# Optimization experiments

Measured on AMD Instinct MI355X. Metric: run time of the kernel, lower is better.

Reference implementation:

```python
import jax, jax.numpy as jnp
import numpy as np

ALPHA = 32.0
RANK = 16
SCALE = ALPHA / RANK


def setup_inputs() -> dict:
    key = jax.random.key(0)
    k1, k2, k3, k4, k5 = jax.random.split(key, 5)
    B, S, D_IN, D_OUT, N = 4, 2048, 4096, 4096, 8
    x = jax.random.normal(k1, (B, S, D_IN), dtype=jnp.float32)
    routing_w = jax.random.uniform(k2, (B, N), dtype=jnp.float32)
    W_base = jax.random.normal(k3, (D_OUT, D_IN), dtype=jnp.float32) * 0.02
    lora_down = jax.random.normal(k4, (N, RANK, D_IN), dtype=jnp.float32) * 0.02
    lora_up = jax.random.normal(k5, (N, D_OUT, RANK), dtype=jnp.float32) * 0.02
    return {"x": x, "routing_w": routing_w, "W_base": W_base,
            "lora_down": lora_down, "lora_up": lora_up}


def reference(x, routing_w, W_base, lora_down, lora_up):
    # base linear: [B,S,D_in] @ [D_out,D_in]^T -> [B,S,D_out]
    base_out = jnp.einsum('bsi,oi->bso', x, W_base)
    # per-expert LoRA down-proj: [B,S,D_in] x [N,R,D_in] -> [B,N,S,R]
    down = jnp.einsum('bsi,nri->bnsr', x, lora_down)
    # up-proj + scale: [B,N,S,R] x [N,D_out,R] -> [B,N,S,D_out]
    up = jnp.einsum('bnsr,nor->bnso', down, lora_up) * SCALE
    # routing-weighted sum over experts: [B,N] x [B,N,S,D_out] -> [B,S,D_out]
    adapter_out = jnp.einsum('bn,bnso->bso', routing_w, up)
    return base_out + adapter_out
```

## Files before the change

kernel.cpp:

```cpp
#include <hip/hip_runtime.h>
#include <hip/hip_bf16.h>
#include <stdint.h>

#define TOK    8192
#define DIN    4096
#define DOUT   4096
#define NEXP   8
#define RK     16
#define NRANK  128
#define KE     4224
#define SEQB   2048
#define LSCALE 2.0f
#define KSPLIT 4
#define KSLICE (DIN / KSPLIT)

typedef __attribute__((ext_vector_type(8))) short bf8_t;
typedef __attribute__((ext_vector_type(4))) float f4_t;

__device__ __forceinline__ void async_copy16(const void* g, void* l) {
  __builtin_amdgcn_global_load_lds((const __attribute__((address_space(1))) void*)g,
                                   (__attribute__((address_space(3))) void*)l,
                                   16, 0, 0);
}

__device__ __forceinline__ ushort f2bf(float f) {
  __hip_bfloat16 h = __float2bfloat16(f);
  return *reinterpret_cast<ushort*>(&h);
}

#define R0 (TOK * DIN / 8)
#define R1 (DOUT * DIN / 8)
#define R2 (DOUT * NEXP * 2)
#define R3 (NRANK * DIN / 8)
#define RTOT (R0 + R1 + R2 + R3)

__global__ __launch_bounds__(256)
void cvt_all_kernel(const float* __restrict__ x, const float* __restrict__ wb,
                    const float* __restrict__ lu, const float* __restrict__ ld,
                    ushort* __restrict__ Xe, ushort* __restrict__ Wc,
                    ushort* __restrict__ Ldb) {
  int i = blockIdx.x * 256 + threadIdx.x;
  const float* src;
  ushort* dst;
  if (i < R0) {
    int t = i >> 9;
    int c = (i & 511) * 8;
    src = x + (size_t)t * DIN + c;
    dst = Xe + (size_t)t * KE + c;
  } else if (i < R0 + R1) {
    int j = i - R0;
    int t = j >> 9;
    int c = (j & 511) * 8;
    src = wb + (size_t)t * DIN + c;
    dst = Wc + (size_t)t * KE + c;
  } else if (i < R0 + R1 + R2) {
    int j = i - (R0 + R1);
    int o = j >> 4;
    int rem = j & 15;
    int n = rem >> 1;
    int half = rem & 1;
    src = lu + ((size_t)n * DOUT + o) * RK + half * 8;
    dst = Wc + (size_t)o * KE + DIN + n * RK + half * 8;
  } else {
    int j = i - (R0 + R1 + R2);
    src = ld + (size_t)j * 8;
    dst = Ldb + (size_t)j * 8;
  }
  const float4* s = reinterpret_cast<const float4*>(src);
  float4 a = s[0], b = s[1];
  union { ushort u[8]; uint4 v; } o;
  o.u[0]=f2bf(a.x); o.u[1]=f2bf(a.y); o.u[2]=f2bf(a.z); o.u[3]=f2bf(a.w);
  o.u[4]=f2bf(b.x); o.u[5]=f2bf(b.y); o.u[6]=f2bf(b.z); o.u[7]=f2bf(b.w);
  *reinterpret_cast<uint4*>(dst) = o.v;
}

template<int KLEN, int LDB, int MODE>
__global__ __launch_bounds__(256)
void gemm128(const ushort* __restrict__ A,
             const ushort* __restrict__ Bm,
             float* __restrict__ C) {
  __shared__ __align__(16) ushort As[128 * 32];
  __shared__ __align__(16) ushort Bs[128 * 32];

  const int tid  = threadIdx.x;
  const int wave = tid >> 6;
  const int lane = tid & 63;

  int bm, bn;
  if (MODE == 0) {
    int bid = blockIdx.x;
    int xcd = bid & 7;
    int idx = bid >> 3;
    int nt  = xcd * 4 + (idx & 3);
    int mt  = idx >> 2;
    bm = mt * 128;
    bn = nt * 128;
  } else {
    bm = blockIdx.y * 128;
    bn = blockIdx.x * 128;
  }
  const int wm = wave & 1, wn = wave >> 1;

  f4_t acc[4][4];
#pragma unroll
  for (int i = 0; i < 4; i++)
#pragma unroll
    for (int j = 0; j < 4; j++) acc[i][j] = (f4_t){0.f, 0.f, 0.f, 0.f};

  const int f0 = tid * 8;
  const int r0 = f0 >> 5, c0 = f0 & 31;
  const int f1 = (256 + tid) * 8;
  const int r1 = f1 >> 5, c1 = f1 & 31;
  const int l0 = (wave << 6) * 8;
  const int l1 = (256 + (wave << 6)) * 8;

  const ushort* Ar = As + (wm * 64 + (lane & 15)) * 32 + (lane >> 4) * 8;
  const ushort* Br = Bs + (wn * 64 + (lane & 15)) * 32 + (lane >> 4) * 8;

  const int kbase = (MODE == 1) ? blockIdx.z * KSLICE : 0;
  const int kend  = kbase + KLEN;

  for (int k0 = kbase; k0 < kend; k0 += 32) {
    __syncthreads();
    async_copy16(A  + (size_t)(bm + r0) * KE  + k0 + c0, (void*)(As + l0));
    async_copy16(A  + (size_t)(bm + r1) * KE  + k0 + c1, (void*)(As + l1));
    async_copy16(Bm + (size_t)(bn + r0) * LDB + k0 + c0, (void*)(Bs + l0));
    async_copy16(Bm + (size_t)(bn + r1) * LDB + k0 + c1, (void*)(Bs + l1));
    __syncthreads();
    bf8_t av[4], bv[4];
#pragma unroll
    for (int i = 0; i < 4; i++) av[i] = *(const bf8_t*)(Ar + i * 16 * 32);
#pragma unroll
    for (int j = 0; j < 4; j++) bv[j] = *(const bf8_t*)(Br + j * 16 * 32);
#pragma unroll
    for (int i = 0; i < 4; i++)
#pragma unroll
      for (int j = 0; j < 4; j++)
        acc[i][j] = __builtin_amdgcn_mfma_f32_16x16x32_bf16(av[i], bv[j], acc[i][j], 0, 0, 0);
  }

  if (MODE == 0) {
#pragma unroll
    for (int i = 0; i < 4; i++) {
      int row = bm + wm * 64 + i * 16 + (lane >> 4) * 4;
#pragma unroll
      for (int j = 0; j < 4; j++) {
        int col = bn + wn * 64 + j * 16 + (lane & 15);
#pragma unroll
        for (int rr = 0; rr < 4; rr++)
          C[(size_t)(row + rr) * DOUT + col] = acc[i][j][rr];
      }
    }
  } else {
    float* Dz = C + (size_t)blockIdx.z * TOK * NRANK;
#pragma unroll
    for (int i = 0; i < 4; i++) {
      int row = bm + wm * 64 + i * 16 + (lane >> 4) * 4;
#pragma unroll
      for (int j = 0; j < 4; j++) {
        int col = wn * 64 + j * 16 + (lane & 15);
#pragma unroll
        for (int rr = 0; rr < 4; rr++)
          Dz[(size_t)(row + rr) * NRANK + col] = acc[i][j][rr];
      }
    }
  }
}

__global__ void scale_store_kernel(const float* __restrict__ D32,
                                   const float* __restrict__ rw,
                                   ushort* __restrict__ Xe) {
  int i = blockIdx.x * 256 + threadIdx.x;
  int t = i >> 5;
  int g = (i & 31) * 4;
  size_t base = (size_t)t * NRANK + g;
  const size_t ss = (size_t)TOK * NRANK;
  float4 a = *reinterpret_cast<const float4*>(D32 + base);
  float4 b = *reinterpret_cast<const float4*>(D32 + ss + base);
  float4 c = *reinterpret_cast<const float4*>(D32 + 2 * ss + base);
  float4 d = *reinterpret_cast<const float4*>(D32 + 3 * ss + base);
  int n = g >> 4;
  int bb = t / SEQB;
  float s = rw[bb * NEXP + n] * LSCALE;
  union { ushort u[4]; uint2 v; } o;
  o.u[0] = f2bf((a.x + b.x + c.x + d.x) * s);
  o.u[1] = f2bf((a.y + b.y + c.y + d.y) * s);
  o.u[2] = f2bf((a.z + b.z + c.z + d.z) * s);
  o.u[3] = f2bf((a.w + b.w + c.w + d.w) * s);
  *reinterpret_cast<uint2*>(Xe + (size_t)t * KE + DIN + g) = o.v;
}

#define BK32  32
#define NT132 (KE / BK32)

__global__ __launch_bounds__(512, 2)
void gemm256(const ushort* __restrict__ A, const ushort* __restrict__ Bm,
             float* __restrict__ C) {
  __shared__ __align__(16) ushort As[4][256 * 32];
  __shared__ __align__(16) ushort Bs[4][256 * 32];

  const int tid  = threadIdx.x;
  const int w    = tid >> 6;
  const int lane = tid & 63;
  const int wm   = w >> 2;
  const int wn   = w & 3;

  const int bid = blockIdx.x;
  const int xg  = bid & 7;
  const int jj  = bid >> 3;
  const int bm  = (((xg & 3) << 3) + (jj & 7)) << 8;
  const int bn  = (((xg >> 2) << 3) + (jj >> 3)) << 8;

  f4_t acc[8][4];
#pragma unroll
  for (int i = 0; i < 8; ++i)
#pragma unroll
    for (int q = 0; q < 4; ++q) acc[i][q] = (f4_t){0.f, 0.f, 0.f, 0.f};

  const int frow = lane & 15;
  const int cbs  = (((lane >> 4) ^ (frow >> 1)) << 4);
  const int ar0  = wm * 128;
  const int br0  = wn * 64;

  const int sxr = (lane >> 3) << 4;
  const int t0  = (w << 10) + (lane << 4);
  const int l0b = t0 ^ sxr;
  const int l1b = (t0 + 8192) ^ sxr;
  const size_t goff0 = (size_t)(l0b >> 6) * KE + ((l0b & 63) >> 1);
  const size_t goff1 = (size_t)(l1b >> 6) * KE + ((l1b & 63) >> 1);
  const int ld0 = (w << 9);
  const int ld1 = (w << 9) + 4096;

  const ushort* Ap = A  + (size_t)bm * KE;
  const ushort* Bp = Bm + (size_t)bn * KE;

#define STAGE_A256(kt, buf) do {                                   \
    const ushort* cp_ = Ap + (size_t)(kt) * BK32;                  \
    async_copy16(cp_ + goff0, (void*)(As[buf] + ld0));             \
    async_copy16(cp_ + goff1, (void*)(As[buf] + ld1));             \
  } while (0)
#define STAGE_B256(kt, buf) do {                                   \
    const ushort* cp_ = Bp + (size_t)(kt) * BK32;                  \
    async_copy16(cp_ + goff0, (void*)(Bs[buf] + ld0));             \
    async_copy16(cp_ + goff1, (void*)(Bs[buf] + ld1));             \
  } while (0)
#define RD_A(s_, mh, f_) (*(const bf8_t*)((const char*)As[s_] + \
    (((ar0 + (mh) * 64 + (f_) * 16 + frow) << 6) ^ cbs)))
#define RD_B(s_, g_) (*(const bf8_t*)((const char*)Bs[s_] + \
    (((br0 + (g_) * 16 + frow) << 6) ^ cbs)))

  STAGE_A256(0, 0); STAGE_B256(0, 0);
  STAGE_A256(1, 1); STAGE_B256(1, 1);
  STAGE_A256(2, 2); STAGE_B256(2, 2);
  asm volatile("s_waitcnt vmcnt(4)" ::: "memory");
  __builtin_amdgcn_s_barrier();

  bf8_t fA0[2][4], fA1[2][4], fB[2][4];
#pragma unroll
  for (int f = 0; f < 4; ++f) fA0[0][f] = RD_A(0, 0, f);
#pragma unroll
  for (int g = 0; g < 4; ++g) fB[0][g]  = RD_B(0, g);

  for (int t2 = 0; t2 < NT132; t2 += 2) {
#pragma unroll
    for (int u = 0; u < 2; ++u) {
      const int T  = t2 + u;
      const int b  = T & 3;
      const int b1 = (T + 1) & 3;
      const int sb = (T + 3) & 3;

      __builtin_amdgcn_s_setprio(1);
#pragma unroll
      for (int f = 0; f < 4; ++f) fA1[u][f] = RD_A(b, 1, f);
      if (T + 3 < NT132) STAGE_A256(T + 3, sb);
#pragma unroll
      for (int f = 0; f < 4; ++f)
#pragma unroll
        for (int g = 0; g < 4; ++g)
          acc[f][g] = __builtin_amdgcn_mfma_f32_16x16x32_bf16(fA0[u][f], fB[u][g], acc[f][g], 0, 0, 0);
      __builtin_amdgcn_s_setprio(0);
      __builtin_amdgcn_s_barrier();

      __builtin_amdgcn_s_setprio(1);
      if (T + 1 < NT132) {
#pragma unroll
        for (int f = 0; f < 4; ++f) fA0[u ^ 1][f] = RD_A(b1, 0, f);
#pragma unroll
        for (int g = 0; g < 4; ++g) fB[u ^ 1][g]  = RD_B(b1, g);
      }
      if (T + 3 < NT132) STAGE_B256(T + 3, sb);
#pragma unroll
      for (int f = 0; f < 4; ++f)
#pragma unroll
        for (int g = 0; g < 4; ++g)
          acc[4 + f][g] = __builtin_amdgcn_mfma_f32_16x16x32_bf16(fA1[u][f], fB[u][g], acc[4 + f][g], 0, 0, 0);
      __builtin_amdgcn_s_setprio(0);
      if (T < NT132 - 4) asm volatile("s_waitcnt vmcnt(4)" ::: "memory");
      else               asm volatile("s_waitcnt vmcnt(0)" ::: "memory");
      __builtin_amdgcn_s_barrier();
    }
  }

#pragma unroll
  for (int i = 0; i < 8; ++i) {
    int row = bm + wm * 128 + i * 16 + (lane >> 4) * 4;
#pragma unroll
    for (int q = 0; q < 4; ++q) {
      int col = bn + wn * 64 + q * 16 + (lane & 15);
#pragma unroll
      for (int rr = 0; rr < 4; ++rr)
        C[(size_t)(row + rr) * DOUT + col] = acc[i][q][rr];
    }
  }
#undef STAGE_A256
#undef STAGE_B256
#undef RD_A
#undef RD_B
}

extern "C" void kernel_launch(void* const* d_in, const int* in_sizes, int n_in,
                              void* d_out, int out_size, void* d_ws, size_t ws_size,
                              hipStream_t stream) {
  const float* x  = (const float*)d_in[0];
  const float* rw = (const float*)d_in[1];
  const float* wb = (const float*)d_in[2];
  const float* ld = (const float*)d_in[3];
  const float* lu = (const float*)d_in[4];
  float* out = (float*)d_out;

  ushort* Xe  = (ushort*)d_ws;
  ushort* Wc  = Xe + (size_t)TOK * KE;
  ushort* Ldb = Wc + (size_t)DOUT * KE;
  float*  D32 = (float*)(Ldb + (size_t)NRANK * DIN);

  cvt_all_kernel<<<RTOT / 256, 256, 0, stream>>>(x, wb, lu, ld, Xe, Wc, Ldb);

  gemm128<KSLICE, DIN, 1><<<dim3(1, TOK / 128, KSPLIT), 256, 0, stream>>>(Xe, Ldb, D32);
  scale_store_kernel<<<TOK * NRANK / 4 / 256, 256, 0, stream>>>(D32, rw, Xe);
  gemm256<<<dim3((TOK / 256) * (DOUT / 256)), 512, 0, stream>>>(Xe, Wc, out);
}
```

Baseline: 558.5 us.

## Fuse x bf16 conversion and split-K reduction into the LoRA down-projection kernel

The fp32 x conversion moves out of the standalone convert kernel and into the down-projection GEMM. That GEMM now loads x as fp32, converts it to bf16 in registers, and writes it both to LDS and to the extended Xe buffer. The separate scale/store kernel is removed: the last split-K block for each row tile, detected with an atomic counter, sums the partials, applies the routing scale and writes the result into Xe. This saves one full pass over x and a kernel launch. In exchange it adds synchronous global loads in the GEMM loop, a memset, and atomic and threadfence synchronisation.

```diff
diff --git a/kernel.cpp b/kernel.cpp
--- a/kernel.cpp
+++ b/kernel.cpp
@@ -28,33 +28,25 @@
   return *reinterpret_cast<ushort*>(&h);
 }
 
-#define R0 (TOK * DIN / 8)
-#define R1 (DOUT * DIN / 8)
-#define R2 (DOUT * NEXP * 2)
-#define R3 (NRANK * DIN / 8)
-#define RTOT (R0 + R1 + R2 + R3)
+#define RR1 (DOUT * DIN / 8)
+#define RR2 (DOUT * NEXP * 2)
+#define RR3 (NRANK * DIN / 8)
+#define RRTOT (RR1 + RR2 + RR3)
 
 __global__ __launch_bounds__(256)
-void cvt_all_kernel(const float* __restrict__ x, const float* __restrict__ wb,
-                    const float* __restrict__ lu, const float* __restrict__ ld,
-                    ushort* __restrict__ Xe, ushort* __restrict__ Wc,
-                    ushort* __restrict__ Ldb) {
+void cvt_rest_kernel(const float* __restrict__ wb, const float* __restrict__ lu,
+                     const float* __restrict__ ld,
+                     ushort* __restrict__ Wc, ushort* __restrict__ Ldb) {
   int i = blockIdx.x * 256 + threadIdx.x;
   const float* src;
   ushort* dst;
-  if (i < R0) {
+  if (i < RR1) {
     int t = i >> 9;
     int c = (i & 511) * 8;
-    src = x + (size_t)t * DIN + c;
-    dst = Xe + (size_t)t * KE + c;
-  } else if (i < R0 + R1) {
-    int j = i - R0;
-    int t = j >> 9;
-    int c = (j & 511) * 8;
     src = wb + (size_t)t * DIN + c;
     dst = Wc + (size_t)t * KE + c;
-  } else if (i < R0 + R1 + R2) {
-    int j = i - (R0 + R1);
+  } else if (i < RR1 + RR2) {
+    int j = i - RR1;
     int o = j >> 4;
     int rem = j & 15;
     int n = rem >> 1;
@@ -62,7 +54,7 @@
     src = lu + ((size_t)n * DOUT + o) * RK + half * 8;
     dst = Wc + (size_t)o * KE + DIN + n * RK + half * 8;
   } else {
-    int j = i - (R0 + R1 + R2);
+    int j = i - (RR1 + RR2);
     src = ld + (size_t)j * 8;
     dst = Ldb + (size_t)j * 8;
   }
@@ -74,31 +66,22 @@
   *reinterpret_cast<uint4*>(dst) = o.v;
 }
 
-template<int KLEN, int LDB, int MODE>
 __global__ __launch_bounds__(256)
-void gemm128(const ushort* __restrict__ A,
-             const ushort* __restrict__ Bm,
-             float* __restrict__ C) {
+void down_fused_kernel(const float* __restrict__ x,
+                       const ushort* __restrict__ Ldb,
+                       float* __restrict__ D32,
+                       ushort* __restrict__ Xe,
+                       const float* __restrict__ rw,
+                       unsigned int* __restrict__ cnt) {
   __shared__ __align__(16) ushort As[128 * 32];
   __shared__ __align__(16) ushort Bs[128 * 32];
 
   const int tid  = threadIdx.x;
   const int wave = tid >> 6;
   const int lane = tid & 63;
-
-  int bm, bn;
-  if (MODE == 0) {
-    int bid = blockIdx.x;
-    int xcd = bid & 7;
-    int idx = bid >> 3;
-    int nt  = xcd * 4 + (idx & 3);
-    int mt  = idx >> 2;
-    bm = mt * 128;
-    bn = nt * 128;
-  } else {
-    bm = blockIdx.y * 128;
-    bn = blockIdx.x * 128;
-  }
+  const int bm   = blockIdx.y * 128;
+  const int z    = blockIdx.z;
+  const int kbase = z * KSLICE;
   const int wm = wave & 1, wn = wave >> 1;
 
   f4_t acc[4][4];
@@ -107,25 +90,35 @@
 #pragma unroll
     for (int j = 0; j < 4; j++) acc[i][j] = (f4_t){0.f, 0.f, 0.f, 0.f};
 
-  const int f0 = tid * 8;
-  const int r0 = f0 >> 5, c0 = f0 & 31;
-  const int f1 = (256 + tid) * 8;
-  const int r1 = f1 >> 5, c1 = f1 & 31;
+  const int r0 = tid >> 2;
+  const int c0 = (tid * 8) & 31;
   const int l0 = (wave << 6) * 8;
   const int l1 = (256 + (wave << 6)) * 8;
 
+  const float*  xr0 = x  + (size_t)(bm + r0)      * DIN + c0;
+  const float*  xr1 = x  + (size_t)(bm + 64 + r0) * DIN + c0;
+  ushort*       xe0 = Xe + (size_t)(bm + r0)      * KE  + c0;
+  ushort*       xe1 = Xe + (size_t)(bm + 64 + r0) * KE  + c0;
+
   const ushort* Ar = As + (wm * 64 + (lane & 15)) * 32 + (lane >> 4) * 8;
   const ushort* Br = Bs + (wn * 64 + (lane & 15)) * 32 + (lane >> 4) * 8;
 
-  const int kbase = (MODE == 1) ? blockIdx.z * KSLICE : 0;
-  const int kend  = kbase + KLEN;
-
-  for (int k0 = kbase; k0 < kend; k0 += 32) {
+  for (int kk = kbase; kk < kbase + KSLICE; kk += 32) {
     __syncthreads();
-    async_copy16(A  + (size_t)(bm + r0) * KE  + k0 + c0, (void*)(As + l0));
-    async_copy16(A  + (size_t)(bm + r1) * KE  + k0 + c1, (void*)(As + l1));
-    async_copy16(Bm + (size_t)(bn + r0) * LDB + k0 + c0, (void*)(Bs + l0));
-    async_copy16(Bm + (size_t)(bn + r1) * LDB + k0 + c1, (void*)(Bs + l1));
+    async_copy16(Ldb + (size_t)r0 * DIN + kk + c0,        (void*)(Bs + l0));
+    async_copy16(Ldb + (size_t)(64 + r0) * DIN + kk + c0, (void*)(Bs + l1));
+    const float4* s0 = reinterpret_cast<const float4*>(xr0 + kk);
+    const float4* s1 = reinterpret_cast<const float4*>(xr1 + kk);
+    float4 pa = s0[0], pb = s0[1], qa = s1[0], qb = s1[1];
+    union { ushort u[8]; uint4 v; } o0, o1;
+    o0.u[0]=f2bf(pa.x); o0.u[1]=f2bf(pa.y); o0.u[2]=f2bf(pa.z); o0.u[3]=f2bf(pa.w);
+    o0.u[4]=f2bf(pb.x); o0.u[5]=f2bf(pb.y); o0.u[6]=f2bf(pb.z); o0.u[7]=f2bf(pb.w);
+    o1.u[0]=f2bf(qa.x); o1.u[1]=f2bf(qa.y); o1.u[2]=f2bf(qa.z); o1.u[3]=f2bf(qa.w);
+    o1.u[4]=f2bf(qb.x); o1.u[5]=f2bf(qb.y); o1.u[6]=f2bf(qb.z); o1.u[7]=f2bf(qb.w);
+    *reinterpret_cast<uint4*>(As + (size_t)tid * 8)        = o0.v;
+    *reinterpret_cast<uint4*>(As + 2048 + (size_t)tid * 8) = o1.v;
+    *reinterpret_cast<uint4*>(xe0 + kk) = o0.v;
+    *reinterpret_cast<uint4*>(xe1 + kk) = o1.v;
     __syncthreads();
     bf8_t av[4], bv[4];
 #pragma unroll
@@ -139,55 +132,47 @@
         acc[i][j] = __builtin_amdgcn_mfma_f32_16x16x32_bf16(av[i], bv[j], acc[i][j], 0, 0, 0);
   }
 
-  if (MODE == 0) {
-#pragma unroll
-    for (int i = 0; i < 4; i++) {
-      int row = bm + wm * 64 + i * 16 + (lane >> 4) * 4;
-#pragma unroll
-      for (int j = 0; j < 4; j++) {
-        int col = bn + wn * 64 + j * 16 + (lane & 15);
-#pragma unroll
-        for (int rr = 0; rr < 4; rr++)
-          C[(size_t)(row + rr) * DOUT + col] = acc[i][j][rr];
-      }
+  float* Dz = D32 + (size_t)z * TOK * NRANK;
+#pragma unroll
+  for (int i = 0; i < 4; i++) {
+    int row = bm + wm * 64 + i * 16 + (lane >> 4) * 4;
+#pragma unroll
+    for (int j = 0; j < 4; j++) {
+      int col = wn * 64 + j * 16 + (lane & 15);
+#pragma unroll
+      for (int rr = 0; rr < 4; rr++)
+        Dz[(size_t)(row + rr) * NRANK + col] = acc[i][j][rr];
     }
-  } else {
-    float* Dz = C + (size_t)blockIdx.z * TOK * NRANK;
-#pragma unroll
-    for (int i = 0; i < 4; i++) {
-      int row = bm + wm * 64 + i * 16 + (lane >> 4) * 4;
-#pragma unroll
-      for (int j = 0; j < 4; j++) {
-        int col = wn * 64 + j * 16 + (lane & 15);
-#pragma unroll
-        for (int rr = 0; rr < 4; rr++)
-          Dz[(size_t)(row + rr) * NRANK + col] = acc[i][j][rr];
-      }
-    }
-  }
-}
-
-__global__ void scale_store_kernel(const float* __restrict__ D32,
-                                   const float* __restrict__ rw,
-                                   ushort* __restrict__ Xe) {
-  int i = blockIdx.x * 256 + threadIdx.x;
-  int t = i >> 5;
-  int g = (i & 31) * 4;
-  size_t base = (size_t)t * NRANK + g;
+  }
+
+  __threadfence();
+  __syncthreads();
+  __shared__ int last_s;
+  if (tid == 0)
+    last_s = (atomicAdd(&cnt[blockIdx.y], 1u) == KSPLIT - 1);
+  __syncthreads();
+  if (!last_s) return;
+  __threadfence();
+
   const size_t ss = (size_t)TOK * NRANK;
-  float4 a = *reinterpret_cast<const float4*>(D32 + base);
-  float4 b = *reinterpret_cast<const float4*>(D32 + ss + base);
-  float4 c = *reinterpret_cast<const float4*>(D32 + 2 * ss + base);
-  float4 d = *reinterpret_cast<const float4*>(D32 + 3 * ss + base);
-  int n = g >> 4;
-  int bb = t / SEQB;
-  float s = rw[bb * NEXP + n] * LSCALE;
-  union { ushort u[4]; uint2 v; } o;
-  o.u[0] = f2bf((a.x + b.x + c.x + d.x) * s);
-  o.u[1] = f2bf((a.y + b.y + c.y + d.y) * s);
-  o.u[2] = f2bf((a.z + b.z + c.z + d.z) * s);
-  o.u[3] = f2bf((a.w + b.w + c.w + d.w) * s);
-  *reinterpret_cast<uint2*>(Xe + (size_t)t * KE + DIN + g) = o.v;
+  for (int it = tid; it < 128 * 32; it += 256) {
+    int t = bm + (it >> 5);
+    int g = (it & 31) * 4;
+    size_t base = (size_t)t * NRANK + g;
+    float4 a = *reinterpret_cast<const float4*>(D32 + base);
+    float4 b = *reinterpret_cast<const float4*>(D32 + ss + base);
+    float4 c = *reinterpret_cast<const float4*>(D32 + 2 * ss + base);
+    float4 d = *reinterpret_cast<const float4*>(D32 + 3 * ss + base);
+    int n = g >> 4;
+    int bb = t / SEQB;
+    float s = rw[bb * NEXP + n] * LSCALE;
+    union { ushort u[4]; uint2 v; } o;
+    o.u[0] = f2bf((a.x + b.x + c.x + d.x) * s);
+    o.u[1] = f2bf((a.y + b.y + c.y + d.y) * s);
+    o.u[2] = f2bf((a.z + b.z + c.z + d.z) * s);
+    o.u[3] = f2bf((a.w + b.w + c.w + d.w) * s);
+    *reinterpret_cast<uint2*>(Xe + (size_t)t * KE + DIN + g) = o.v;
+  }
 }
 
 #define BK32  32
@@ -332,10 +317,14 @@
   ushort* Wc  = Xe + (size_t)TOK * KE;
   ushort* Ldb = Wc + (size_t)DOUT * KE;
   float*  D32 = (float*)(Ldb + (size_t)NRANK * DIN);
-
-  cvt_all_kernel<<<RTOT / 256, 256, 0, stream>>>(x, wb, lu, ld, Xe, Wc, Ldb);
-
-  gemm128<KSLICE, DIN, 1><<<dim3(1, TOK / 128, KSPLIT), 256, 0, stream>>>(Xe, Ldb, D32);
-  scale_store_kernel<<<TOK * NRANK / 4 / 256, 256, 0, stream>>>(D32, rw, Xe);
+  unsigned int* cnt = (unsigned int*)(D32 + (size_t)KSPLIT * TOK * NRANK);
+
+  hipMemsetAsync(cnt, 0, (TOK / 128) * sizeof(unsigned int), stream);
+
+  cvt_rest_kernel<<<RRTOT / 256, 256, 0, stream>>>(wb, lu, ld, Wc, Ldb);
+
+  down_fused_kernel<<<dim3(1, TOK / 128, KSPLIT), 256, 0, stream>>>(
+      x, Ldb, D32, Xe, rw, cnt);
+
   gemm256<<<dim3((TOK / 256) * (DOUT / 256)), 512, 0, stream>>>(Xe, Wc, out);
 }
```

Result: slower. 616.8 us (+10.4%).

## Fuse LoRA down-proj split-K reduction and scaling via atomics and last-block epilogue

Applied to the files above, without the earlier changes.

The down-projection split-K grows from 4 to 16 slices, so 1024 blocks are launched instead of 256. Partial results are now accumulated with atomicAdd into a single zeroed fp32 buffer instead of four separate slices. A per-row-tile counter picks the last finishing block, which applies routing scale and bf16 conversion into the extended activation buffer, so the separate scale_store kernel is removed. This costs two memsets, float atomics with nondeterministic summation order, and a threadfence/counter handshake.

```diff
diff --git a/kernel.cpp b/kernel.cpp
--- a/kernel.cpp
+++ b/kernel.cpp
@@ -11,7 +11,7 @@
 #define KE     4224
 #define SEQB   2048
 #define LSCALE 2.0f
-#define KSPLIT 4
+#define KSPLIT 16
 #define KSLICE (DIN / KSPLIT)
 
 typedef __attribute__((ext_vector_type(8))) short bf8_t;
@@ -74,31 +74,20 @@
   *reinterpret_cast<uint4*>(dst) = o.v;
 }
 
-template<int KLEN, int LDB, int MODE>
 __global__ __launch_bounds__(256)
-void gemm128(const ushort* __restrict__ A,
-             const ushort* __restrict__ Bm,
-             float* __restrict__ C) {
+void down_k16_kernel(const ushort* __restrict__ A,
+                     const ushort* __restrict__ Bm,
+                     float* __restrict__ D32,
+                     ushort* __restrict__ Xe,
+                     const float* __restrict__ rw,
+                     unsigned int* __restrict__ cnt) {
   __shared__ __align__(16) ushort As[128 * 32];
   __shared__ __align__(16) ushort Bs[128 * 32];
 
   const int tid  = threadIdx.x;
   const int wave = tid >> 6;
   const int lane = tid & 63;
-
-  int bm, bn;
-  if (MODE == 0) {
-    int bid = blockIdx.x;
-    int xcd = bid & 7;
-    int idx = bid >> 3;
-    int nt  = xcd * 4 + (idx & 3);
-    int mt  = idx >> 2;
-    bm = mt * 128;
-    bn = nt * 128;
-  } else {
-    bm = blockIdx.y * 128;
-    bn = blockIdx.x * 128;
-  }
+  const int bm   = blockIdx.y * 128;
   const int wm = wave & 1, wn = wave >> 1;
 
   f4_t acc[4][4];
@@ -117,15 +106,15 @@
   const ushort* Ar = As + (wm * 64 + (lane & 15)) * 32 + (lane >> 4) * 8;
   const ushort* Br = Bs + (wn * 64 + (lane & 15)) * 32 + (lane >> 4) * 8;
 
-  const int kbase = (MODE == 1) ? blockIdx.z * KSLICE : 0;
-  const int kend  = kbase + KLEN;
+  const int kbase = blockIdx.z * KSLICE;
+  const int kend  = kbase + KSLICE;
 
   for (int k0 = kbase; k0 < kend; k0 += 32) {
     __syncthreads();
     async_copy16(A  + (size_t)(bm + r0) * KE  + k0 + c0, (void*)(As + l0));
     async_copy16(A  + (size_t)(bm + r1) * KE  + k0 + c1, (void*)(As + l1));
-    async_copy16(Bm + (size_t)(bn + r0) * LDB + k0 + c0, (void*)(Bs + l0));
-    async_copy16(Bm + (size_t)(bn + r1) * LDB + k0 + c1, (void*)(Bs + l1));
+    async_copy16(Bm + (size_t)r0 * DIN + k0 + c0, (void*)(Bs + l0));
+    async_copy16(Bm + (size_t)r1 * DIN + k0 + c1, (void*)(Bs + l1));
     __syncthreads();
     bf8_t av[4], bv[4];
 #pragma unroll
@@ -139,55 +128,41 @@
         acc[i][j] = __builtin_amdgcn_mfma_f32_16x16x32_bf16(av[i], bv[j], acc[i][j], 0, 0, 0);
   }
 
-  if (MODE == 0) {
-#pragma unroll
-    for (int i = 0; i < 4; i++) {
-      int row = bm + wm * 64 + i * 16 + (lane >> 4) * 4;
-#pragma unroll
-      for (int j = 0; j < 4; j++) {
-        int col = bn + wn * 64 + j * 16 + (lane & 15);
-#pragma unroll
-        for (int rr = 0; rr < 4; rr++)
-          C[(size_t)(row + rr) * DOUT + col] = acc[i][j][rr];
-      }
+#pragma unroll
+  for (int i = 0; i < 4; i++) {
+    int row = bm + wm * 64 + i * 16 + (lane >> 4) * 4;
+#pragma unroll
+    for (int j = 0; j < 4; j++) {
+      int col = wn * 64 + j * 16 + (lane & 15);
+#pragma unroll
+      for (int rr = 0; rr < 4; rr++)
+        atomicAdd(&D32[(size_t)(row + rr) * NRANK + col], acc[i][j][rr]);
     }
-  } else {
-    float* Dz = C + (size_t)blockIdx.z * TOK * NRANK;
-#pragma unroll
-    for (int i = 0; i < 4; i++) {
-      int row = bm + wm * 64 + i * 16 + (lane >> 4) * 4;
-#pragma unroll
-      for (int j = 0; j < 4; j++) {
-        int col = wn * 64 + j * 16 + (lane & 15);
-#pragma unroll
-        for (int rr = 0; rr < 4; rr++)
-          Dz[(size_t)(row + rr) * NRANK + col] = acc[i][j][rr];
-      }
-    }
-  }
-}
-
-__global__ void scale_store_kernel(const float* __restrict__ D32,
-                                   const float* __restrict__ rw,
-                                   ushort* __restrict__ Xe) {
-  int i = blockIdx.x * 256 + threadIdx.x;
-  int t = i >> 5;
-  int g = (i & 31) * 4;
-  size_t base = (size_t)t * NRANK + g;
-  const size_t ss = (size_t)TOK * NRANK;
-  float4 a = *reinterpret_cast<const float4*>(D32 + base);
-  float4 b = *reinterpret_cast<const float4*>(D32 + ss + base);
-  float4 c = *reinterpret_cast<const float4*>(D32 + 2 * ss + base);
-  float4 d = *reinterpret_cast<const float4*>(D32 + 3 * ss + base);
-  int n = g >> 4;
-  int bb = t / SEQB;
-  float s = rw[bb * NEXP + n] * LSCALE;
-  union { ushort u[4]; uint2 v; } o;
-  o.u[0] = f2bf((a.x + b.x + c.x + d.x) * s);
-  o.u[1] = f2bf((a.y + b.y + c.y + d.y) * s);
-  o.u[2] = f2bf((a.z + b.z + c.z + d.z) * s);
-  o.u[3] = f2bf((a.w + b.w + c.w + d.w) * s);
-  *reinterpret_cast<uint2*>(Xe + (size_t)t * KE + DIN + g) = o.v;
+  }
+
+  __threadfence();
+  __syncthreads();
+  __shared__ int last_s;
+  if (tid == 0)
+    last_s = (atomicAdd(&cnt[blockIdx.y], 1u) == KSPLIT - 1);
+  __syncthreads();
+  if (!last_s) return;
+  __threadfence();
+
+  for (int it = tid; it < 128 * 32; it += 256) {
+    int t = bm + (it >> 5);
+    int g = (it & 31) * 4;
+    float4 a = *reinterpret_cast<const float4*>(D32 + (size_t)t * NRANK + g);
+    int n = g >> 4;
+    int bb = t / SEQB;
+    float s = rw[bb * NEXP + n] * LSCALE;
+    union { ushort u[4]; uint2 v; } o;
+    o.u[0] = f2bf(a.x * s);
+    o.u[1] = f2bf(a.y * s);
+    o.u[2] = f2bf(a.z * s);
+    o.u[3] = f2bf(a.w * s);
+    *reinterpret_cast<uint2*>(Xe + (size_t)t * KE + DIN + g) = o.v;
+  }
 }
 
 #define BK32  32
@@ -332,10 +307,15 @@
   ushort* Wc  = Xe + (size_t)TOK * KE;
   ushort* Ldb = Wc + (size_t)DOUT * KE;
   float*  D32 = (float*)(Ldb + (size_t)NRANK * DIN);
+  unsigned int* cnt = (unsigned int*)(D32 + (size_t)TOK * NRANK);
+
+  hipMemsetAsync(D32, 0, (size_t)TOK * NRANK * sizeof(float), stream);
+  hipMemsetAsync(cnt, 0, (TOK / 128) * sizeof(unsigned int), stream);
 
   cvt_all_kernel<<<RTOT / 256, 256, 0, stream>>>(x, wb, lu, ld, Xe, Wc, Ldb);
 
-  gemm128<KSLICE, DIN, 1><<<dim3(1, TOK / 128, KSPLIT), 256, 0, stream>>>(Xe, Ldb, D32);
-  scale_store_kernel<<<TOK * NRANK / 4 / 256, 256, 0, stream>>>(D32, rw, Xe);
+  down_k16_kernel<<<dim3(1, TOK / 128, KSPLIT), 256, 0, stream>>>(
+      Xe, Ldb, D32, Xe, rw, cnt);
+
   gemm256<<<dim3((TOK / 256) * (DOUT / 256)), 512, 0, stream>>>(Xe, Wc, out);
 }
```

Result: slower. 682.2 us (+22.1%).
